# Kernel tuning notes

Measured on AMD Instinct MI355X. Metric: run time of the kernel, lower is better.

## Reference

```python
import jax, jax.numpy as jnp
import numpy as np

NF = 64            # nf_effect
N_HISTORY = 3
ADJ_THRESH = 0.12  # float adj_thresh passed to construct_edges
PSTEP = 3


def _relu(x):
    return jnp.maximum(x, 0)


def construct_edges(states, thresh, mask, tool_mask, topk):
    """JAX port of construct_edges_from_states_batch (connect_tools_all=False).
    Returns fixed-shape Rr, Rs of shape (B, N*topk, N); each receiver i owns
    slots [i*topk, (i+1)*topk). Invalid slots are all-zero rows, which is
    math-equivalent to torch's compacted n_rel under all bmms.
    """
    B, N, _ = states.shape
    dt = states.dtype
    d = states[:, :, None, :] - states[:, None, :, :]          # (B,N,N,3)
    dis = jnp.sum(d * d, axis=-1)                              # (B,N,N)
    big = jnp.asarray(1e10, dt)
    m12 = mask[:, :, None] & mask[:, None, :]                  # valid pair
    t12 = tool_mask[:, :, None] & tool_mask[:, None, :]        # tool-tool: cut
    dis = jnp.where(m12 & ~t12, dis, big)
    adj = dis < (thresh * thresh)                              # (B,N,N) bool
    # connect_tools_all=False branch: zero tool-receiver / obj-sender edges
    adj = adj & ~(tool_mask[:, :, None] & mask[:, None, :])
    _, idx = jax.lax.top_k(-dis, topk)                         # (B,N,topk) smallest dis
    valid = jnp.take_along_axis(adj, idx, axis=-1).astype(dt)  # (B,N,topk)
    recv_oh = jnp.eye(N, dtype=dt)                             # (N,N)
    Rr = (valid[..., None] * recv_oh[None, :, None, :]).reshape(B, N * topk, N)
    Rs = (valid[..., None] * jax.nn.one_hot(idx, N, dtype=dt)).reshape(B, N * topk, N)
    return Rr, Rs


def _prop_forward(states, a_cur, s_delta, Rr, Rs,
                  pe_w1, pe_b1, pe_w2, pe_b2,
                  re_w1, re_b1, re_w2, re_b2, re_w3, re_b3,
                  rp_w, rp_b, pp_w, pp_b,
                  pr_w1, pr_b1, pr_w2, pr_b2):
    # s_delta: (B, 3*n_history, N) -> (B, N, 3*n_history)
    s_delta_flat = jnp.transpose(s_delta, (0, 2, 1))
    nh = N_HISTORY
    # relation features: receiver/sender attrs + position difference
    a_r = jnp.einsum('brn,bn->br', Rr, a_cur)[..., None]       # (B,R,1)
    a_s = jnp.einsum('brn,bn->br', Rs, a_cur)[..., None]
    s_r = jnp.einsum('brn,bnd->brd', Rr, states)               # (B,R,3)
    s_s = jnp.einsum('brn,bnd->brd', Rs, states)
    rel_in = jnp.concatenate([a_r, a_s, s_r - s_s], axis=-1)   # (B,R,5)
    # relation encoder: 3-layer MLP, ReLU after each
    h = _relu(rel_in @ re_w1 + re_b1)
    h = _relu(h @ re_w2 + re_b2)
    rel_enc = _relu(h @ re_w3 + re_b3)                         # (B,R,NF)
    # particle encoder: [s_delta history | attrs tiled n_history] -> 12 dims
    p_in = jnp.concatenate(
        [s_delta_flat, jnp.repeat(a_cur[..., None], nh, axis=-1)], axis=-1)
    p_enc = _relu(_relu(p_in @ pe_w1 + pe_b1) @ pe_w2 + pe_b2)  # (B,N,NF)
    effect = p_enc
    for _ in range(PSTEP):
        eff_r = jnp.einsum('brn,bnd->brd', Rr, effect)
        eff_s = jnp.einsum('brn,bnd->brd', Rs, effect)
        rel_eff = _relu(
            jnp.concatenate([rel_enc, eff_r, eff_s], axis=-1) @ rp_w + rp_b)
        agg = jnp.einsum('brn,brd->bnd', Rr, rel_eff)          # Rr^T bmm
        effect = _relu(
            jnp.concatenate([p_enc, agg], axis=-1) @ pp_w + pp_b + effect)
    pred = _relu(effect @ pr_w1 + pr_b1) @ pr_w2 + pr_b2       # (B,N,3)
    return states + pred  # add_delta=True


def setup_inputs():
    key = jax.random.key(0)
    ks = jax.random.split(key, 16)
    B, N = 2, 2048
    states = jax.random.uniform(ks[0], (B, N, 3), dtype=jnp.float32)
    a_cur = jax.random.uniform(ks[1], (B, N), dtype=jnp.float32)
    s_delta = jax.random.normal(ks[2], (B, 3 * N_HISTORY, N), dtype=jnp.float32) * 0.01
    mask = jnp.ones((B, N), dtype=bool)
    tool_mask = jnp.broadcast_to(jnp.arange(N) < N // 20, (B, N))
    s = lambda fan: 1.0 / np.sqrt(fan)
    p = lambda k, sh: jax.random.normal(k, sh, dtype=jnp.float32) * s(sh[0])
    z = lambda n: jnp.zeros((n,), dtype=jnp.float32)
    params = {
        'pe_w1': p(ks[3], (4 * N_HISTORY, NF)), 'pe_b1': z(NF),
        'pe_w2': p(ks[4], (NF, NF)), 'pe_b2': z(NF),
        're_w1': p(ks[5], (5, NF)), 're_b1': z(NF),
        're_w2': p(ks[6], (NF, NF)), 're_b2': z(NF),
        're_w3': p(ks[7], (NF, NF)), 're_b3': z(NF),
        'rp_w': p(ks[8], (3 * NF, NF)), 'rp_b': z(NF),
        'pp_w': p(ks[9], (2 * NF, NF)), 'pp_b': z(NF),
        'pr_w1': p(ks[10], (NF, NF)), 'pr_b1': z(NF),
        'pr_w2': p(ks[11], (NF, 3)), 'pr_b2': z(3),
    }
    return {'states': states, 'a_cur': a_cur, 's_delta': s_delta,
            'mask': mask, 'tool_mask': tool_mask, 'topk': 8, **params}


def reference(states, a_cur, s_delta, mask, tool_mask, topk,
              pe_w1, pe_b1, pe_w2, pe_b2,
              re_w1, re_b1, re_w2, re_b2, re_w3, re_b3,
              rp_w, rp_b, pp_w, pp_b,
              pr_w1, pr_b1, pr_w2, pr_b2):
    Rr, Rs = construct_edges(states, ADJ_THRESH, mask, tool_mask, topk)
    return _prop_forward(states, a_cur, s_delta, Rr, Rs,
                         pe_w1, pe_b1, pe_w2, pe_b2,
                         re_w1, re_b1, re_w2, re_b2, re_w3, re_b3,
                         rp_w, rp_b, pp_w, pp_b,
                         pr_w1, pr_b1, pr_w2, pr_b2)
```

## Files before the change

### kernel.cpp

```cpp
#include <hip/hip_runtime.h>
#include <math.h>

#define DEV __device__ __forceinline__

constexpr int BB = 2, N = 2048, KK = 8;
constexpr int NODES = BB * N;
constexpr int NSLOTS = NODES * KK;
constexpr int NPB = 8;
constexpr int TPB = 512;
constexpr int NBLK = NODES / NPB;

DEV int bool_mode(const void* p) {
  unsigned v = *(const unsigned*)p;
  if (v == 0x3f800000u) return 2;
  if (v <= 1u) return 1;
  return 0;
}
DEV bool read_mask(const void* p, int i, int mode) {
  if (mode == 2) return ((const float*)p)[i] != 0.f;
  if (mode == 1) return ((const int*)p)[i] != 0;
  return ((const unsigned char*)p)[i] != 0;
}

DEV void mv8(float* acc, const float* __restrict__ W, const float* act, int col) {
  #pragma unroll 4
  for (int k = 0; k < 64; ++k) {
    float hk = act[k * 65 + col];
    #pragma unroll
    for (int u = 0; u < 8; ++u) acc[u] = fmaf(hk, W[k * 64 + u], acc[u]);
  }
}
DEV void stage8(float* act, int col, int f0, const float* t) {
  #pragma unroll
  for (int u = 0; u < 8; ++u) act[(f0 + u) * 65 + col] = t[u];
}
DEV void load8(float* t, const float* __restrict__ g) {
  float4 v0 = ((const float4*)g)[0], v1 = ((const float4*)g)[1];
  t[0] = v0.x; t[1] = v0.y; t[2] = v0.z; t[3] = v0.w;
  t[4] = v1.x; t[5] = v1.y; t[6] = v1.z; t[7] = v1.w;
}
DEV void store8(float* __restrict__ g, const float* t) {
  ((float4*)g)[0] = make_float4(t[0], t[1], t[2], t[3]);
  ((float4*)g)[1] = make_float4(t[4], t[5], t[6], t[7]);
}

#define LESS(da, ja, db, jb) ((da) < (db) || ((da) == (db) && (ja) < (jb)))
#define CE(a, b)                                                              \
  {                                                                           \
    bool sw_ = LESS(nd[b], nj[b], nd[a], nj[a]);                              \
    float t_ = nd[a]; int u_ = nj[a];                                         \
    if (sw_) { nd[a] = nd[b]; nj[a] = nj[b]; nd[b] = t_; nj[b] = u_; }        \
  }

struct SEdge { float px[N], py[N], pz[N], padd[N]; };
struct SMlp  { float act[64 * 65]; };
union SU { SEdge e; SMlp m; };

__global__ __launch_bounds__(TPB, 4) void k_front(
    const float* __restrict__ states, const void* maskp, const void* toolp,
    const float* __restrict__ a_cur, const float* __restrict__ s_delta,
    const float* __restrict__ pe_w1, const float* __restrict__ pe_b1,
    const float* __restrict__ pe_w2, const float* __restrict__ pe_b2,
    const float* __restrict__ re_w1, const float* __restrict__ re_b1,
    const float* __restrict__ re_w2, const float* __restrict__ re_b2,
    const float* __restrict__ re_w3, const float* __restrict__ re_b3,
    const float* __restrict__ rp_w, const float* __restrict__ rp_b,
    const float* __restrict__ pp_w, const float* __restrict__ pp_b,
    int* __restrict__ eidx, float* __restrict__ evalid,
    float* __restrict__ p_const, float* __restrict__ rel_const,
    float* __restrict__ eff0) {
  __shared__ SU sm;
  __shared__ int   sl_idx[64];
  __shared__ float sl_val[64];
  const int tid = threadIdx.x;
  const int wav = tid >> 6, lane = tid & 63;
  const int blk = blockIdx.x;
  const int node0 = blk * NPB;
  const int b = node0 >> 11;
  const int mm = bool_mode(maskp), mt = bool_mode(toolp);

  {
    for (int j = tid; j < N; j += TPB) {
      const float* s = states + (size_t)(b * N + j) * 3;
      sm.e.px[j] = s[0]; sm.e.py[j] = s[1]; sm.e.pz[j] = s[2];
      sm.e.padd[j] = read_mask(maskp, b * N + j, mm) ? 0.f : 1e10f;
    }
    __syncthreads();
    const int node = node0 + wav;
    const int i = node & (N - 1);
    const bool mi = read_mask(maskp, node, mm);
    const bool ti = read_mask(toolp, node, mt);
    float td[KK]; int tj[KK];
    #pragma unroll
    for (int k = 0; k < KK; ++k) { td[k] = 3.0e38f; tj[k] = 0; }
    if (mi && !ti) {
      const float sx = sm.e.px[i], sy = sm.e.py[i], sz = sm.e.pz[i];
      #pragma unroll 4
      for (int it = 0; it < N / 64; ++it) {
        int j = lane + it * 64;
        float dx = sx - sm.e.px[j], dy = sy - sm.e.py[j], dz = sz - sm.e.pz[j];
        float dis = __fadd_rn(__fadd_rn(__fmul_rn(dx, dx), __fmul_rn(dy, dy)),
                              __fmul_rn(dz, dz));
        float dd = __fadd_rn(dis, sm.e.padd[j]);
        if (dd < td[KK - 1]) {
          float cd = dd; int cj = j;
          #pragma unroll
          for (int m = 0; m < KK; ++m) {
            bool sw = cd < td[m];
            float od = td[m]; int oj = tj[m];
            td[m] = sw ? cd : od; tj[m] = sw ? cj : oj;
            cd = sw ? od : cd;   cj = sw ? oj : cj;
          }
        }
      }
      #pragma unroll
      for (int m = 1; m < 64; m <<= 1) {
        float pd[KK]; int pj[KK];
        #pragma unroll
        for (int r = 0; r < KK; ++r) {
          pd[r] = __shfl_xor(td[r], m);
          pj[r] = __shfl_xor(tj[r], m);
        }
        float nd[KK]; int nj[KK];
        #pragma unroll
        for (int r = 0; r < KK; ++r) {
          float ad = td[r]; int aj = tj[r];
          float bd = pd[KK - 1 - r]; int bj = pj[KK - 1 - r];
          bool tb = LESS(bd, bj, ad, aj);
          nd[r] = tb ? bd : ad; nj[r] = tb ? bj : aj;
        }
        CE(0, 4) CE(1, 5) CE(2, 6) CE(3, 7)
        CE(0, 2) CE(1, 3) CE(4, 6) CE(5, 7)
        CE(0, 1) CE(2, 3) CE(4, 5) CE(6, 7)
        #pragma unroll
        for (int r = 0; r < KK; ++r) { td[r] = nd[r]; tj[r] = nj[r]; }
      }
    }
    if (lane == 0) {
      const float T2 = (float)(0.12 * 0.12);
      const bool ok = mi && !ti;
      #pragma unroll
      for (int k = 0; k < KK; ++k) {
        float v = (ok && td[k] < T2) ? 1.f : 0.f;
        sl_idx[wav * KK + k] = tj[k];
        sl_val[wav * KK + k] = v;
        eidx[node * KK + k] = tj[k];
        evalid[node * KK + k] = v;
      }
    }
    __syncthreads();
  }

  {
    float* hb = sm.m.act;
    const int nd = node0 + wav;
    const int i = nd & (N - 1);
    const int f = lane;
    float sd[9];
    #pragma unroll
    for (int k = 0; k < 9; ++k) sd[k] = s_delta[(b * 9 + k) * N + i];
    const float a = a_cur[nd];
    float x = pe_b1[f];
    #pragma unroll
    for (int k = 0; k < 9; ++k) x = fmaf(sd[k], pe_w1[k * 64 + f], x);
    x = fmaf(a, pe_w1[576 + f] + pe_w1[640 + f] + pe_w1[704 + f], x);
    x = fmaxf(x, 0.f);
    hb[f * 9 + wav] = x;
    __syncthreads();
    float y = pe_b2[f];
    #pragma unroll 4
    for (int k = 0; k < 64; ++k) y = fmaf(hb[k * 9 + wav], pe_w2[k * 64 + f], y);
    y = fmaxf(y, 0.f);
    eff0[(size_t)nd * 64 + f] = y;
    __syncthreads();
    hb[f * 9 + wav] = y;
    __syncthreads();
    float z = pp_b[f];
    #pragma unroll 4
    for (int k = 0; k < 64; ++k) z = fmaf(hb[k * 9 + wav], pp_w[k * 64 + f], z);
    p_const[(size_t)nd * 64 + f] = z;
    __syncthreads();
  }

  {
    float* act = sm.m.act;
    const int f0 = __builtin_amdgcn_readfirstlane(wav * 8);
    const int col = lane;
    const int slot = blk * 64 + col;
    const int nd = node0 + (col >> 3);
    const int nb = nd & ~(N - 1);
    const int j = nb + sl_idx[col];
    const float a_r = a_cur[nd], a_s = a_cur[j];
    const float dx = states[nd * 3]     - states[j * 3];
    const float dy = states[nd * 3 + 1] - states[j * 3 + 1];
    const float dz = states[nd * 3 + 2] - states[j * 3 + 2];
    float t[8];
    #pragma unroll
    for (int u = 0; u < 8; ++u) {
      const int f = f0 + u;
      float x = re_b1[f];
      x = fmaf(a_r, re_w1[f], x);
      x = fmaf(a_s, re_w1[64 + f], x);
      x = fmaf(dx, re_w1[128 + f], x);
      x = fmaf(dy, re_w1[192 + f], x);
      x = fmaf(dz, re_w1[256 + f], x);
      t[u] = fmaxf(x, 0.f);
    }
    stage8(act, col, f0, t);
    __syncthreads();
    #pragma unroll
    for (int u = 0; u < 8; ++u) t[u] = re_b2[f0 + u];
    mv8(t, re_w2 + f0, act, col);
    #pragma unroll
    for (int u = 0; u < 8; ++u) t[u] = fmaxf(t[u], 0.f);
    __syncthreads();
    stage8(act, col, f0, t);
    __syncthreads();
    #pragma unroll
    for (int u = 0; u < 8; ++u) t[u] = re_b3[f0 + u];
    mv8(t, re_w3 + f0, act, col);
    #pragma unroll
    for (int u = 0; u < 8; ++u) t[u] = fmaxf(t[u], 0.f);
    __syncthreads();
    stage8(act, col, f0, t);
    __syncthreads();
    #pragma unroll
    for (int u = 0; u < 8; ++u) t[u] = rp_b[f0 + u];
    mv8(t, rp_w + f0, act, col);
    const float v = sl_val[col];
    #pragma unroll
    for (int u = 0; u < 8; ++u) t[u] *= v;
    store8(rel_const + (size_t)slot * 64 + f0, t);
  }
}

template <int HEAD>
__global__ __launch_bounds__(TPB, 4) void k_prop(
    const float* __restrict__ rp_w, const float* __restrict__ pp_w,
    const int* __restrict__ eidx, const float* __restrict__ evalid,
    const float* __restrict__ p_const, const float* __restrict__ rel_const,
    const float* __restrict__ effIn, float* __restrict__ effOut,
    const float* __restrict__ states,
    const float* __restrict__ pr_w1, const float* __restrict__ pr_b1,
    const float* __restrict__ pr_w2, const float* __restrict__ pr_b2,
    float* __restrict__ out) {
  __shared__ float act[64 * 65];
  __shared__ float agg[64 * 9];
  const int tid = threadIdx.x;
  const int wav = tid >> 6, lane = tid & 63;
  const int blk = blockIdx.x;
  const int node0 = blk * NPB;
  const int f0 = __builtin_amdgcn_readfirstlane(wav * 8);
  const int col = lane;
  const int slot = blk * 64 + col;
  const int nd = node0 + (col >> 3);
  const int nb = nd & ~(N - 1);
  const int j = nb + eidx[slot];
  float r[8];
  load8(r, effIn + (size_t)nd * 64 + f0);
  stage8(act, col, f0, r);
  __syncthreads();
  float t[8];
  load8(t, rel_const + (size_t)slot * 64 + f0);
  mv8(t, rp_w + 4096 + f0, act, col);
  __syncthreads();
  load8(r, effIn + (size_t)j * 64 + f0);
  stage8(act, col, f0, r);
  __syncthreads();
  mv8(t, rp_w + 8192 + f0, act, col);
  const float v = evalid[slot];
  #pragma unroll
  for (int u = 0; u < 8; ++u) {
    float x = fmaxf(t[u], 0.f) * v;
    x += __shfl_xor(x, 1);
    x += __shfl_xor(x, 2);
    x += __shfl_xor(x, 4);
    t[u] = x;
  }
  {
    const int e = col & 7, n = col >> 3;
    float val = t[0];
    #pragma unroll
    for (int u = 1; u < 8; ++u) val = (e == u) ? t[u] : val;
    agg[(f0 + e) * 9 + n] = val;
  }
  __syncthreads();
  const int onode = node0 + wav;
  float o = p_const[(size_t)onode * 64 + lane];
  #pragma unroll 4
  for (int g = 0; g < 64; ++g)
    o = fmaf(agg[g * 9 + wav], pp_w[4096 + g * 64 + lane], o);
  const float er = effIn[(size_t)onode * 64 + lane];
  const float ov = fmaxf(o + er, 0.f);
  if (HEAD == 0) {
    effOut[(size_t)onode * 64 + lane] = ov;
  } else {
    __syncthreads();
    agg[lane * 9 + wav] = ov;
    __syncthreads();
    float h = pr_b1[lane];
    #pragma unroll 4
    for (int k = 0; k < 64; ++k)
      h = fmaf(agg[k * 9 + wav], pr_w1[k * 64 + lane], h);
    h = fmaxf(h, 0.f);
    float p0 = h * pr_w2[lane * 3];
    float p1 = h * pr_w2[lane * 3 + 1];
    float p2 = h * pr_w2[lane * 3 + 2];
    #pragma unroll
    for (int m = 1; m < 64; m <<= 1) {
      p0 += __shfl_xor(p0, m);
      p1 += __shfl_xor(p1, m);
      p2 += __shfl_xor(p2, m);
    }
    if (lane == 0) {
      out[onode * 3]     = states[onode * 3]     + p0 + pr_b2[0];
      out[onode * 3 + 1] = states[onode * 3 + 1] + p1 + pr_b2[1];
      out[onode * 3 + 2] = states[onode * 3 + 2] + p2 + pr_b2[2];
    }
  }
}

extern "C" void kernel_launch(void* const* d_in, const int* in_sizes, int n_in,
                              void* d_out, int out_size, void* d_ws, size_t ws_size,
                              hipStream_t stream) {
  const float* states  = (const float*)d_in[0];
  const float* a_cur   = (const float*)d_in[1];
  const float* s_delta = (const float*)d_in[2];
  const void*  maskp   = d_in[3];
  const void*  toolp   = d_in[4];
  const float* pe_w1 = (const float*)d_in[6];
  const float* pe_b1 = (const float*)d_in[7];
  const float* pe_w2 = (const float*)d_in[8];
  const float* pe_b2 = (const float*)d_in[9];
  const float* re_w1 = (const float*)d_in[10];
  const float* re_b1 = (const float*)d_in[11];
  const float* re_w2 = (const float*)d_in[12];
  const float* re_b2 = (const float*)d_in[13];
  const float* re_w3 = (const float*)d_in[14];
  const float* re_b3 = (const float*)d_in[15];
  const float* rp_w  = (const float*)d_in[16];
  const float* rp_b  = (const float*)d_in[17];
  const float* pp_w  = (const float*)d_in[18];
  const float* pp_b  = (const float*)d_in[19];
  const float* pr_w1 = (const float*)d_in[20];
  const float* pr_b1 = (const float*)d_in[21];
  const float* pr_w2 = (const float*)d_in[22];
  const float* pr_b2 = (const float*)d_in[23];

  char* w = (char*)d_ws;
  int*   eidx      = (int*)w;   w += (size_t)NSLOTS * 4;
  float* evalid    = (float*)w; w += (size_t)NSLOTS * 4;
  float* p_const   = (float*)w; w += (size_t)NODES * 64 * 4;
  float* rel_const = (float*)w; w += (size_t)NSLOTS * 64 * 4;
  float* effA      = (float*)w; w += (size_t)NODES * 64 * 4;
  float* effB      = (float*)w; w += (size_t)NODES * 64 * 4;
  float* out       = (float*)d_out;

  k_front<<<NBLK, TPB, 0, stream>>>(states, maskp, toolp, a_cur, s_delta,
      pe_w1, pe_b1, pe_w2, pe_b2, re_w1, re_b1, re_w2, re_b2, re_w3, re_b3,
      rp_w, rp_b, pp_w, pp_b, eidx, evalid, p_const, rel_const, effA);
  k_prop<0><<<NBLK, TPB, 0, stream>>>(rp_w, pp_w, eidx, evalid, p_const,
      rel_const, effA, effB, states, pr_w1, pr_b1, pr_w2, pr_b2, out);
  k_prop<0><<<NBLK, TPB, 0, stream>>>(rp_w, pp_w, eidx, evalid, p_const,
      rel_const, effB, effA, states, pr_w1, pr_b1, pr_w2, pr_b2, out);
  k_prop<1><<<NBLK, TPB, 0, stream>>>(rp_w, pp_w, eidx, evalid, p_const,
      rel_const, effA, effB, states, pr_w1, pr_b1, pr_w2, pr_b2, out);
}
```

Baseline: 191.8 us.

## Run edge MLPs on bf16 MFMA with swizzled LDS tiles

Replaces the scalar fp32 per-edge 64x64 matrix-vector loops in both the front and propagation kernels with bf16 MFMA 16x16x32 tiles. Weights are transposed and packed to bf16 in swizzled LDS, and activations are staged as bf16 rows. The goal is to cut the FMA-bound edge MLP cost by using the matrix cores. The trade-offs are bf16 rounding error, extra per-block weight staging, and more LDS use per block.

```diff
diff --git a/kernel.cpp b/kernel.cpp
--- a/kernel.cpp
+++ b/kernel.cpp
@@ -10,6 +10,10 @@
 constexpr int TPB = 512;
 constexpr int NBLK = NODES / NPB;
 
+typedef __attribute__((ext_vector_type(8))) short short8v;
+typedef __attribute__((ext_vector_type(4))) float float4v;
+union S8 { short8v v; unsigned u[4]; unsigned short s[8]; };
+
 DEV int bool_mode(const void* p) {
   unsigned v = *(const unsigned*)p;
   if (v == 0x3f800000u) return 2;
@@ -22,26 +26,33 @@
   return ((const unsigned char*)p)[i] != 0;
 }
 
-DEV void mv8(float* acc, const float* __restrict__ W, const float* act, int col) {
-  #pragma unroll 4
-  for (int k = 0; k < 64; ++k) {
-    float hk = act[k * 65 + col];
-    #pragma unroll
-    for (int u = 0; u < 8; ++u) acc[u] = fmaf(hk, W[k * 64 + u], acc[u]);
-  }
-}
-DEV void stage8(float* act, int col, int f0, const float* t) {
+DEV unsigned short f2bf(float x) {
+  unsigned u = __builtin_bit_cast(unsigned, x);
+  return (unsigned short)((u + 0x7FFFu + ((u >> 16) & 1u)) >> 16);
+}
+DEV unsigned pk2(float a, float b) {
+  return (unsigned)f2bf(a) | ((unsigned)f2bf(b) << 16);
+}
+
+DEV short8v rdA(const unsigned short* T, int row, int kk0) {
+  return *(const short8v*)&T[row * 64 + (kk0 ^ ((row & 7) << 3))];
+}
+DEV void stage_wT(const float* __restrict__ W, unsigned short* wt, int t) {
+  const int f = t & 63, k0 = (t >> 6) * 8;
+  S8 p;
   #pragma unroll
-  for (int u = 0; u < 8; ++u) act[(f0 + u) * 65 + col] = t[u];
-}
-DEV void load8(float* t, const float* __restrict__ g) {
-  float4 v0 = ((const float4*)g)[0], v1 = ((const float4*)g)[1];
-  t[0] = v0.x; t[1] = v0.y; t[2] = v0.z; t[3] = v0.w;
-  t[4] = v1.x; t[5] = v1.y; t[6] = v1.z; t[7] = v1.w;
-}
-DEV void store8(float* __restrict__ g, const float* t) {
-  ((float4*)g)[0] = make_float4(t[0], t[1], t[2], t[3]);
-  ((float4*)g)[1] = make_float4(t[4], t[5], t[6], t[7]);
+  for (int q = 0; q < 4; ++q)
+    p.u[q] = pk2(W[(k0 + 2 * q) * 64 + f], W[(k0 + 2 * q + 1) * 64 + f]);
+  *(short8v*)&wt[f * 64 + (k0 ^ ((f & 7) << 3))] = p.v;
+}
+DEV void stage_row8(unsigned short* T, int row, int kq, const float* __restrict__ g) {
+  const int k0 = kq * 8;
+  float4 v0 = ((const float4*)(g + k0))[0];
+  float4 v1 = ((const float4*)(g + k0))[1];
+  S8 p;
+  p.u[0] = pk2(v0.x, v0.y); p.u[1] = pk2(v0.z, v0.w);
+  p.u[2] = pk2(v1.x, v1.y); p.u[3] = pk2(v1.z, v1.w);
+  *(short8v*)&T[row * 64 + (k0 ^ ((row & 7) << 3))] = p.v;
 }
 
 #define LESS(da, ja, db, jb) ((da) < (db) || ((da) == (db) && (ja) < (jb)))
@@ -53,8 +64,8 @@
   }
 
 struct SEdge { float px[N], py[N], pz[N], padd[N]; };
-struct SMlp  { float act[64 * 65]; };
-union SU { SEdge e; SMlp m; };
+struct SMlpF { unsigned short A0[4096]; unsigned short A1[4096]; float hb[64 * 9]; };
+union SUF { SEdge e; SMlpF m; };
 
 __global__ __launch_bounds__(TPB, 4) void k_front(
     const float* __restrict__ states, const void* maskp, const void* toolp,
@@ -69,21 +80,27 @@
     int* __restrict__ eidx, float* __restrict__ evalid,
     float* __restrict__ p_const, float* __restrict__ rel_const,
     float* __restrict__ eff0) {
-  __shared__ SU sm;
+  __shared__ SUF su;
+  __shared__ unsigned short wt3[3][4096];
   __shared__ int   sl_idx[64];
   __shared__ float sl_val[64];
   const int tid = threadIdx.x;
   const int wav = tid >> 6, lane = tid & 63;
   const int blk = blockIdx.x;
   const int node0 = blk * NPB;
+  const int slot0 = blk * 64;
   const int b = node0 >> 11;
   const int mm = bool_mode(maskp), mt = bool_mode(toolp);
+
+  stage_wT(re_w2, wt3[0], tid);
+  stage_wT(re_w3, wt3[1], tid);
+  stage_wT(rp_w,  wt3[2], tid);
 
   {
     for (int j = tid; j < N; j += TPB) {
       const float* s = states + (size_t)(b * N + j) * 3;
-      sm.e.px[j] = s[0]; sm.e.py[j] = s[1]; sm.e.pz[j] = s[2];
-      sm.e.padd[j] = read_mask(maskp, b * N + j, mm) ? 0.f : 1e10f;
+      su.e.px[j] = s[0]; su.e.py[j] = s[1]; su.e.pz[j] = s[2];
+      su.e.padd[j] = read_mask(maskp, b * N + j, mm) ? 0.f : 1e10f;
     }
     __syncthreads();
     const int node = node0 + wav;
@@ -94,14 +111,14 @@
     #pragma unroll
     for (int k = 0; k < KK; ++k) { td[k] = 3.0e38f; tj[k] = 0; }
     if (mi && !ti) {
-      const float sx = sm.e.px[i], sy = sm.e.py[i], sz = sm.e.pz[i];
+      const float sx = su.e.px[i], sy = su.e.py[i], sz = su.e.pz[i];
       #pragma unroll 4
       for (int it = 0; it < N / 64; ++it) {
         int j = lane + it * 64;
-        float dx = sx - sm.e.px[j], dy = sy - sm.e.py[j], dz = sz - sm.e.pz[j];
+        float dx = sx - su.e.px[j], dy = sy - su.e.py[j], dz = sz - su.e.pz[j];
         float dis = __fadd_rn(__fadd_rn(__fmul_rn(dx, dx), __fmul_rn(dy, dy)),
                               __fmul_rn(dz, dz));
-        float dd = __fadd_rn(dis, sm.e.padd[j]);
+        float dd = __fadd_rn(dis, su.e.padd[j]);
         if (dd < td[KK - 1]) {
           float cd = dd; int cj = j;
           #pragma unroll
@@ -144,15 +161,15 @@
         float v = (ok && td[k] < T2) ? 1.f : 0.f;
         sl_idx[wav * KK + k] = tj[k];
         sl_val[wav * KK + k] = v;
-        eidx[node * KK + k] = tj[k];
-        evalid[node * KK + k] = v;
+        eidx[(node0 + wav) * KK + k] = tj[k];
+        evalid[(node0 + wav) * KK + k] = v;
       }
     }
     __syncthreads();
   }
 
   {
-    float* hb = sm.m.act;
+    float* hb = su.m.hb;
     const int nd = node0 + wav;
     const int i = nd & (N - 1);
     const int f = lane;
@@ -183,10 +200,10 @@
   }
 
   {
-    float* act = sm.m.act;
+    unsigned short* A0 = su.m.A0;
+    unsigned short* A1 = su.m.A1;
     const int f0 = __builtin_amdgcn_readfirstlane(wav * 8);
     const int col = lane;
-    const int slot = blk * 64 + col;
     const int nd = node0 + (col >> 3);
     const int nb = nd & ~(N - 1);
     const int j = nb + sl_idx[col];
@@ -206,31 +223,79 @@
       x = fmaf(dz, re_w1[256 + f], x);
       t[u] = fmaxf(x, 0.f);
     }
-    stage8(act, col, f0, t);
-    __syncthreads();
-    #pragma unroll
-    for (int u = 0; u < 8; ++u) t[u] = re_b2[f0 + u];
-    mv8(t, re_w2 + f0, act, col);
-    #pragma unroll
-    for (int u = 0; u < 8; ++u) t[u] = fmaxf(t[u], 0.f);
-    __syncthreads();
-    stage8(act, col, f0, t);
-    __syncthreads();
-    #pragma unroll
-    for (int u = 0; u < 8; ++u) t[u] = re_b3[f0 + u];
-    mv8(t, re_w3 + f0, act, col);
-    #pragma unroll
-    for (int u = 0; u < 8; ++u) t[u] = fmaxf(t[u], 0.f);
-    __syncthreads();
-    stage8(act, col, f0, t);
-    __syncthreads();
-    #pragma unroll
-    for (int u = 0; u < 8; ++u) t[u] = rp_b[f0 + u];
-    mv8(t, rp_w + f0, act, col);
-    const float v = sl_val[col];
-    #pragma unroll
-    for (int u = 0; u < 8; ++u) t[u] *= v;
-    store8(rel_const + (size_t)slot * 64 + f0, t);
+    #pragma unroll
+    for (int u = 0; u < 8; u += 2) {
+      int idx = col * 64 + ((f0 + u) ^ ((col & 7) << 3));
+      *(unsigned*)&A0[idx] = pk2(t[u], t[u + 1]);
+    }
+    __syncthreads();
+
+    const int m = wav & 3, h = wav >> 2;
+    const int n0t = 2 * h, n1t = n0t + 1;
+    const int rowA = m * 16 + (lane & 15);
+    const int fc0 = n0t * 16 + (lane & 15), fc1 = n1t * 16 + (lane & 15);
+    const unsigned long long vm = __ballot(sl_val[lane] != 0.f);
+
+    {
+      float b0 = re_b2[fc0], b1 = re_b2[fc1];
+      float4v c0 = {b0, b0, b0, b0}, c1 = {b1, b1, b1, b1};
+      #pragma unroll
+      for (int ks = 0; ks < 2; ++ks) {
+        const int kk0 = ks * 32 + (lane >> 4) * 8;
+        short8v a  = rdA(A0, rowA, kk0);
+        short8v w0 = rdA(wt3[0], fc0, kk0);
+        short8v w1 = rdA(wt3[0], fc1, kk0);
+        c0 = __builtin_amdgcn_mfma_f32_16x16x32_bf16(a, w0, c0, 0, 0, 0);
+        c1 = __builtin_amdgcn_mfma_f32_16x16x32_bf16(a, w1, c1, 0, 0, 0);
+      }
+      #pragma unroll
+      for (int r = 0; r < 4; ++r) {
+        int slot = m * 16 + (lane >> 4) * 4 + r;
+        A1[slot * 64 + (fc0 ^ ((slot & 7) << 3))] = f2bf(fmaxf(c0[r], 0.f));
+        A1[slot * 64 + (fc1 ^ ((slot & 7) << 3))] = f2bf(fmaxf(c1[r], 0.f));
+      }
+    }
+    __syncthreads();
+    {
+      float b0 = re_b3[fc0], b1 = re_b3[fc1];
+      float4v c0 = {b0, b0, b0, b0}, c1 = {b1, b1, b1, b1};
+      #pragma unroll
+      for (int ks = 0; ks < 2; ++ks) {
+        const int kk0 = ks * 32 + (lane >> 4) * 8;
+        short8v a  = rdA(A1, rowA, kk0);
+        short8v w0 = rdA(wt3[1], fc0, kk0);
+        short8v w1 = rdA(wt3[1], fc1, kk0);
+        c0 = __builtin_amdgcn_mfma_f32_16x16x32_bf16(a, w0, c0, 0, 0, 0);
+        c1 = __builtin_amdgcn_mfma_f32_16x16x32_bf16(a, w1, c1, 0, 0, 0);
+      }
+      #pragma unroll
+      for (int r = 0; r < 4; ++r) {
+        int slot = m * 16 + (lane >> 4) * 4 + r;
+        A0[slot * 64 + (fc0 ^ ((slot & 7) << 3))] = f2bf(fmaxf(c0[r], 0.f));
+        A0[slot * 64 + (fc1 ^ ((slot & 7) << 3))] = f2bf(fmaxf(c1[r], 0.f));
+      }
+    }
+    __syncthreads();
+    {
+      float b0 = rp_b[fc0], b1 = rp_b[fc1];
+      float4v c0 = {b0, b0, b0, b0}, c1 = {b1, b1, b1, b1};
+      #pragma unroll
+      for (int ks = 0; ks < 2; ++ks) {
+        const int kk0 = ks * 32 + (lane >> 4) * 8;
+        short8v a  = rdA(A0, rowA, kk0);
+        short8v w0 = rdA(wt3[2], fc0, kk0);
+        short8v w1 = rdA(wt3[2], fc1, kk0);
+        c0 = __builtin_amdgcn_mfma_f32_16x16x32_bf16(a, w0, c0, 0, 0, 0);
+        c1 = __builtin_amdgcn_mfma_f32_16x16x32_bf16(a, w1, c1, 0, 0, 0);
+      }
+      #pragma unroll
+      for (int r = 0; r < 4; ++r) {
+        int slot = m * 16 + (lane >> 4) * 4 + r;
+        float v = (float)((vm >> slot) & 1ull);
+        rel_const[(size_t)(slot0 + slot) * 64 + fc0] = c0[r] * v;
+        rel_const[(size_t)(slot0 + slot) * 64 + fc1] = c1[r] * v;
+      }
+    }
   }
 }
 
@@ -244,68 +309,97 @@
     const float* __restrict__ pr_w1, const float* __restrict__ pr_b1,
     const float* __restrict__ pr_w2, const float* __restrict__ pr_b2,
     float* __restrict__ out) {
-  __shared__ float act[64 * 65];
-  __shared__ float agg[64 * 9];
+  __shared__ unsigned short AS[4096];
+  __shared__ unsigned short EN[512];
+  __shared__ unsigned short wt2[2][4096];
+  __shared__ float agg[8 * 64];
   const int tid = threadIdx.x;
   const int wav = tid >> 6, lane = tid & 63;
   const int blk = blockIdx.x;
   const int node0 = blk * NPB;
-  const int f0 = __builtin_amdgcn_readfirstlane(wav * 8);
-  const int col = lane;
-  const int slot = blk * 64 + col;
-  const int nd = node0 + (col >> 3);
-  const int nb = nd & ~(N - 1);
-  const int j = nb + eidx[slot];
-  float r[8];
-  load8(r, effIn + (size_t)nd * 64 + f0);
-  stage8(act, col, f0, r);
+  const int slot0 = blk * 64;
+  const int nb = node0 & ~(N - 1);
+
+  stage_wT(rp_w + 4096, wt2[0], tid);
+  stage_wT(rp_w + 8192, wt2[1], tid);
+  {
+    const int slot = tid >> 3, kq = tid & 7;
+    const int j = nb + eidx[slot0 + slot];
+    stage_row8(AS, slot, kq, effIn + (size_t)j * 64);
+  }
+  if (tid < 64) {
+    const int n = tid >> 3, kq = tid & 7;
+    stage_row8(EN, n, kq, effIn + (size_t)(node0 + n) * 64);
+  }
+  const unsigned long long vm = __ballot(evalid[slot0 + lane] != 0.f);
   __syncthreads();
-  float t[8];
-  load8(t, rel_const + (size_t)slot * 64 + f0);
-  mv8(t, rp_w + 4096 + f0, act, col);
+
+  {
+    const int m = wav & 3, h = wav >> 2;
+    const int n0t = 2 * h, n1t = n0t + 1;
+    const int rowA = m * 16 + (lane & 15);
+    const int nodeR = rowA >> 3;
+    const int fc0 = n0t * 16 + (lane & 15), fc1 = n1t * 16 + (lane & 15);
+    float4v c0, c1;
+    #pragma unroll
+    for (int r = 0; r < 4; ++r) {
+      int slot = m * 16 + (lane >> 4) * 4 + r;
+      c0[r] = rel_const[(size_t)(slot0 + slot) * 64 + fc0];
+      c1[r] = rel_const[(size_t)(slot0 + slot) * 64 + fc1];
+    }
+    #pragma unroll
+    for (int ks = 0; ks < 2; ++ks) {
+      const int kk0 = ks * 32 + (lane >> 4) * 8;
+      short8v aR = rdA(EN, nodeR, kk0);
+      short8v aS = rdA(AS, rowA, kk0);
+      short8v w10 = rdA(wt2[0], fc0, kk0);
+      short8v w11 = rdA(wt2[0], fc1, kk0);
+      short8v w20 = rdA(wt2[1], fc0, kk0);
+      short8v w21 = rdA(wt2[1], fc1, kk0);
+      c0 = __builtin_amdgcn_mfma_f32_16x16x32_bf16(aR, w10, c0, 0, 0, 0);
+      c1 = __builtin_amdgcn_mfma_f32_16x16x32_bf16(aR, w11, c1, 0, 0, 0);
+      c0 = __builtin_amdgcn_mfma_f32_16x16x32_bf16(aS, w20, c0, 0, 0, 0);
+      c1 = __builtin_amdgcn_mfma_f32_16x16x32_bf16(aS, w21, c1, 0, 0, 0);
+    }
+    float s0 = 0.f, s1 = 0.f;
+    #pragma unroll
+    for (int r = 0; r < 4; ++r) {
+      int slot = m * 16 + (lane >> 4) * 4 + r;
+      float v = (float)((vm >> slot) & 1ull);
+      s0 += fmaxf(c0[r], 0.f) * v;
+      s1 += fmaxf(c1[r], 0.f) * v;
+    }
+    s0 += __shfl_xor(s0, 16);
+    s1 += __shfl_xor(s1, 16);
+    if (((lane >> 4) & 1) == 0) {
+      const int an = m * 2 + (lane >> 5);
+      agg[an * 64 + fc0] = s0;
+      agg[an * 64 + fc1] = s1;
+    }
+  }
   __syncthreads();
-  load8(r, effIn + (size_t)j * 64 + f0);
-  stage8(act, col, f0, r);
-  __syncthreads();
-  mv8(t, rp_w + 8192 + f0, act, col);
-  const float v = evalid[slot];
-  #pragma unroll
-  for (int u = 0; u < 8; ++u) {
-    float x = fmaxf(t[u], 0.f) * v;
-    x += __shfl_xor(x, 1);
-    x += __shfl_xor(x, 2);
-    x += __shfl_xor(x, 4);
-    t[u] = x;
-  }
-  {
-    const int e = col & 7, n = col >> 3;
-    float val = t[0];
-    #pragma unroll
-    for (int u = 1; u < 8; ++u) val = (e == u) ? t[u] : val;
-    agg[(f0 + e) * 9 + n] = val;
-  }
-  __syncthreads();
+
   const int onode = node0 + wav;
   float o = p_const[(size_t)onode * 64 + lane];
   #pragma unroll 4
   for (int g = 0; g < 64; ++g)
-    o = fmaf(agg[g * 9 + wav], pp_w[4096 + g * 64 + lane], o);
+    o = fmaf(agg[wav * 64 + g], pp_w[4096 + g * 64 + lane], o);
   const float er = effIn[(size_t)onode * 64 + lane];
   const float ov = fmaxf(o + er, 0.f);
   if (HEAD == 0) {
     effOut[(size_t)onode * 64 + lane] = ov;
   } else {
     __syncthreads();
-    agg[lane * 9 + wav] = ov;
-    __syncthreads();
-    float h = pr_b1[lane];
+    agg[wav * 64 + lane] = ov;
+    __syncthreads();
+    float hh = pr_b1[lane];
     #pragma unroll 4
     for (int k = 0; k < 64; ++k)
-      h = fmaf(agg[k * 9 + wav], pr_w1[k * 64 + lane], h);
-    h = fmaxf(h, 0.f);
-    float p0 = h * pr_w2[lane * 3];
-    float p1 = h * pr_w2[lane * 3 + 1];
-    float p2 = h * pr_w2[lane * 3 + 2];
+      hh = fmaf(agg[wav * 64 + k], pr_w1[k * 64 + lane], hh);
+    hh = fmaxf(hh, 0.f);
+    float p0 = hh * pr_w2[lane * 3];
+    float p1 = hh * pr_w2[lane * 3 + 1];
+    float p2 = hh * pr_w2[lane * 3 + 2];
     #pragma unroll
     for (int m = 1; m < 64; m <<= 1) {
       p0 += __shfl_xor(p0, m);
```

New measurement: 161.8 us. -15.7%, faster.
